# Kernel optimization log

Measured on AMD Instinct MI355X. Metric: run time of the kernel, lower is better.

## Reference

```python
import jax, jax.numpy as jnp
import numpy as np

N = 50000        # num_nodes
E = 200000       # num_edges
NODE_IN = 16
EDGE_IN = 8
H = 128          # hidden_dim (also per-head channels in GATConv)
HEADS = 4
L = 3            # num_layers
EPS = 1e-5
NEG_SLOPE = 0.2  # PyG GATConv default


def layer_norm(x, g, b):
    mu = jnp.mean(x, axis=-1, keepdims=True)
    v = jnp.var(x, axis=-1, keepdims=True)
    return (x - mu) * jax.lax.rsqrt(v + EPS) * g + b


def batch_norm_eval(x, g, b, rm, rv):
    return (x - rm) * jax.lax.rsqrt(rv + EPS) * g + b


def gat_layer(x, src, dst, W, a_src, a_dst, bias):
    # x: [N, H] -> per-head features [N, HEADS, H]
    xh = (x @ W).reshape(N, HEADS, H)
    al_src = jnp.sum(xh * a_src, axis=-1)  # [N, HEADS]
    al_dst = jnp.sum(xh * a_dst, axis=-1)  # [N, HEADS]
    alpha = jax.nn.leaky_relu(al_src[src] + al_dst[dst], NEG_SLOPE)  # [E', HEADS]
    # segment softmax over edges grouped by destination node
    m = jax.ops.segment_max(alpha, dst, num_segments=N)
    e = jnp.exp(alpha - m[dst])
    s = jax.ops.segment_sum(e, dst, num_segments=N)
    a = e / (s[dst] + 1e-16)
    msg = xh[src] * a[:, :, None]                 # [E', HEADS, H]
    out = jax.ops.segment_sum(msg, dst, num_segments=N)  # [N, HEADS, H]
    return jnp.mean(out, axis=1) + bias           # concat=False -> head mean


def setup_inputs() -> dict:
    key = jax.random.key(0)
    ks = jax.random.split(key, 24)
    s = 0.1
    inp = {
        "x": jax.random.normal(ks[0], (N, NODE_IN), jnp.float32),
        "edge_index": jax.random.randint(ks[1], (2, E), 0, N, jnp.int32),
        "edge_attr": jax.random.normal(ks[2], (E, EDGE_IN), jnp.float32),
        "shock_mask_nodes": jax.random.randint(ks[3], (N,), 0, 2, jnp.int32),
        # node encoder
        "enc_w": jax.random.normal(ks[4], (NODE_IN + 2, H), jnp.float32) * s,
        "enc_b": jnp.zeros((H,), jnp.float32),
        "enc_ln_g": jnp.ones((H,), jnp.float32),
        "enc_ln_b": jnp.zeros((H,), jnp.float32),
        # GAT layers (stacked over L)
        "gat_w": jax.random.normal(ks[5], (L, H, HEADS * H), jnp.float32) * s,
        "gat_att_src": jax.random.normal(ks[6], (L, HEADS, H), jnp.float32) * s,
        "gat_att_dst": jax.random.normal(ks[7], (L, HEADS, H), jnp.float32) * s,
        "gat_bias": jnp.zeros((L, H), jnp.float32),
        # BatchNorm (eval mode: running stats)
        "bn_g": jnp.ones((L, H), jnp.float32),
        "bn_b": jnp.zeros((L, H), jnp.float32),
        "bn_mean": jax.random.normal(ks[8], (L, H), jnp.float32) * 0.01,
        "bn_var": jnp.ones((L, H), jnp.float32),
        # edge MLP: (2H + EDGE_IN) -> H -> H//2 -> 1
        "em1_w": jax.random.normal(ks[9], (2 * H + EDGE_IN, H), jnp.float32) * s,
        "em1_b": jnp.zeros((H,), jnp.float32),
        "em_ln_g": jnp.ones((H,), jnp.float32),
        "em_ln_b": jnp.zeros((H,), jnp.float32),
        "em2_w": jax.random.normal(ks[10], (H, H // 2), jnp.float32) * s,
        "em2_b": jnp.zeros((H // 2,), jnp.float32),
        "em3_w": jax.random.normal(ks[11], (H // 2, 1), jnp.float32) * s,
        "em3_b": jnp.zeros((1,), jnp.float32),
    }
    return inp


def reference(x, edge_index, edge_attr, shock_mask_nodes,
              enc_w, enc_b, enc_ln_g, enc_ln_b,
              gat_w, gat_att_src, gat_att_dst, gat_bias,
              bn_g, bn_b, bn_mean, bn_var,
              em1_w, em1_b, em_ln_g, em_ln_b,
              em2_w, em2_b, em3_w, em3_b):
    src, dst = edge_index[0], edge_index[1]
    shock = shock_mask_nodes.astype(jnp.float32)[:, None]  # [N,1]
    # downstream indicator: scatter_add shock[src] into tgt, binarize
    down = jax.ops.segment_sum(shock[src, 0], dst, num_segments=N)
    down = (down > 0).astype(jnp.float32)[:, None]
    xa = jnp.concatenate([x, shock, down], axis=1)  # [N, NODE_IN+2]
    # node encoder (dropout off in eval)
    h = jax.nn.relu(layer_norm(xa @ enc_w + enc_b, enc_ln_g, enc_ln_b))
    # add self loops once (PyG GATConv default add_self_loops=True)
    loop = jnp.arange(N, dtype=src.dtype)
    src_sl = jnp.concatenate([src, loop])
    dst_sl = jnp.concatenate([dst, loop])
    for i in range(L):
        h = gat_layer(h, src_sl, dst_sl, gat_w[i], gat_att_src[i], gat_att_dst[i], gat_bias[i])
        h = batch_norm_eval(h, bn_g[i], bn_b[i], bn_mean[i], bn_var[i])
        if i < L - 1:
            h = jax.nn.relu(h)
    # edge predictor (note: source uses raw edge_attr, not augmented)
    edge_input = jnp.concatenate([h[src], h[dst], edge_attr], axis=1)  # [E, 2H+EDGE_IN]
    z = jax.nn.relu(layer_norm(edge_input @ em1_w + em1_b, em_ln_g, em_ln_b))
    z = jax.nn.relu(z @ em2_w + em2_b)
    delta = (z @ em3_w + em3_b)[:, 0]  # [E]
    return delta
```

## Files before the change

### kernel.cpp

```cpp
#include <hip/hip_runtime.h>
#include <hip/hip_bf16.h>


#define N_NODES 50000
#define N_EDGES 200000
#define ETOT    (N_EDGES + N_NODES)
#define HID     128
#define LN_EPS  1e-5f
#define NEG     0.2f
#define NSB     196

typedef __hip_bfloat16 bf16;
typedef __attribute__((ext_vector_type(8))) short v8s;
typedef __attribute__((ext_vector_type(4))) float v4f;
#define MFMA(a, b, c) __builtin_amdgcn_mfma_f32_16x16x32_bf16(a, b, c, 0, 0, 0)

__device__ __forceinline__ float b2f(unsigned short s) {
    return __uint_as_float(((unsigned int)s) << 16);
}
__device__ __forceinline__ unsigned short f2b(float f) {
    __hip_bfloat16 h = __float2bfloat16(f);
    return *reinterpret_cast<unsigned short*>(&h);
}
__device__ __forceinline__ unsigned int pack2(float a, float b) {
    return (unsigned int)f2b(a) | ((unsigned int)f2b(b) << 16);
}
__device__ __forceinline__ float pread(const void* p, size_t i, int isbf) {
    if (isbf) return b2f(((const unsigned short*)p)[i]);
    return ((const float*)p)[i];
}

__global__ void k_fill(float* out, int n, float v) {
    int i = blockIdx.x * blockDim.x + threadIdx.x;
    if (i < n) out[i] = v;
}

__global__ void k_detect(const unsigned short* __restrict__ xbuf,
                         int* __restrict__ flag) {
    int sane = 0;
    for (int j = threadIdx.x; j < 4096; j += 64) {
        unsigned short v = xbuf[2 * j];
        int e = (v >> 7) & 0xFF;
        if (v == 0 || (e > 96 && e < 160)) sane++;
    }
    for (int off = 32; off > 0; off >>= 1) sane += __shfl_down(sane, off);
    if (threadIdx.x == 0) flag[0] = (sane * 10 >= 4096 * 9) ? 1 : 0;
}

struct PrepArgs {
    const void *encw, *encb, *enlg, *enlb, *gatw, *asrc, *adst, *bias,
               *bng, *bnb, *bnm, *bnv, *em1w, *em1b, *emlg, *emlb,
               *em2w, *em2b, *em3w, *em3b;
};
#define PREP_ITEMS (150000 + 8193 + 1024 + 196608 + 32768 + 8192 + 3072 + 6144)
__global__ void k_prep(PrepArgs a, float* __restrict__ pool,
                       unsigned short* __restrict__ gwt,
                       unsigned short* __restrict__ uvt,
                       unsigned short* __restrict__ w2t,
                       float* __restrict__ wl,
                       unsigned short* __restrict__ wlhi,
                       unsigned short* __restrict__ wllo,
                       float* __restrict__ down, int* __restrict__ deg,
                       int* __restrict__ fill, const int* __restrict__ flag) {
    int i = blockIdx.x * 256 + threadIdx.x;
    int bf = flag[0];
    if (i < 150000) {
        int which = i / 50000, idx = i - which * 50000;
        if (which == 0) down[idx] = 0.f;
        else if (which == 1) deg[idx] = 0;
        else fill[idx] = 0;
        return;
    }
    i -= 150000;
    if (i < 8193) {
        const void* s; int off;
        if      (i < 2304) { s = a.encw; off = 0;    }
        else if (i < 2432) { s = a.encb; off = 2304; }
        else if (i < 2560) { s = a.enlg; off = 2432; }
        else if (i < 2688) { s = a.enlb; off = 2560; }
        else if (i < 4224) { s = a.asrc; off = 2688; }
        else if (i < 5760) { s = a.adst; off = 4224; }
        else if (i < 6144) { s = a.bias; off = 5760; }
        else if (i < 6528) { s = a.bng;  off = 6144; }
        else if (i < 6912) { s = a.bnb;  off = 6528; }
        else if (i < 7296) { s = a.bnm;  off = 6912; }
        else if (i < 7680) { s = a.bnv;  off = 7296; }
        else if (i < 7808) { s = a.em1b; off = 7680; }
        else if (i < 7936) { s = a.emlg; off = 7808; }
        else if (i < 8064) { s = a.emlb; off = 7936; }
        else if (i < 8128) { s = a.em2b; off = 8064; }
        else if (i < 8192) { s = a.em3w; off = 8128; }
        else               { s = a.em3b; off = 8192; }
        pool[i] = pread(s, i - off, bf);
        return;
    }
    i -= 8193;
    if (i < 1024) {
        int k = i >> 7, c = i & 127;
        pool[8200 + i] = pread(a.em1w, (size_t)(256 + k) * 128 + c, bf);
        return;
    }
    i -= 1024;
    if (i < 196608) {
        int L = i >> 16, rem = i & 65535, c = rem >> 9, k = rem & 511;
        gwt[i] = f2b(pread(a.gatw,
            (size_t)L * 65536 + (size_t)(k & 127) * 512 + (k >> 7) * 128 + c, bf));
        return;
    }
    i -= 196608;
    if (i < 32768) {
        int n = i >> 7, k = i & 127;
        float v = (n < 128) ? pread(a.em1w, (size_t)k * 128 + n, bf)
                            : pread(a.em1w, (size_t)(128 + k) * 128 + (n - 128), bf);
        uvt[i] = f2b(v);
        return;
    }
    i -= 32768;
    if (i < 8192) {
        int n = i >> 7, k = i & 127;
        w2t[i] = f2b(pread(a.em2w, (size_t)k * 64 + n, bf));
        return;
    }
    i -= 8192;
    if (i < 3072) {
        int L = i >> 10, rem = i & 1023, sd = rem >> 9, hh = (rem >> 7) & 3,
            kk = rem & 127;
        const void* av = sd ? a.adst : a.asrc;
        float acc = 0.f;
        for (int c = 0; c < 128; c++)
            acc += pread(a.gatw,
                       (size_t)L * 65536 + (size_t)kk * 512 + hh * 128 + c, bf)
                 * pread(av, (size_t)L * 512 + hh * 128 + c, bf);
        wl[i] = acc;
        return;
    }
    i -= 3072;
    if (i < 6144) {
        int L = i >> 11, rem = i & 2047, j = rem >> 7, kk = rem & 127;
        float d = 0.f;
        if (j < 8) {
            int sd = j >> 2, hh = j & 3;
            const void* av = sd ? a.adst : a.asrc;
            for (int c = 0; c < 128; c++)
                d += pread(a.gatw,
                         (size_t)L * 65536 + (size_t)kk * 512 + hh * 128 + c, bf)
                   * pread(av, (size_t)L * 512 + hh * 128 + c, bf);
        }
        unsigned short hi = f2b(d);
        wlhi[i] = hi;
        wllo[i] = f2b(d - b2f(hi));
    }
}

__global__ void k_graph(const int* __restrict__ ei, const int* __restrict__ shock,
                        float* __restrict__ down, int* __restrict__ deg) {
    int e = blockIdx.x * blockDim.x + threadIdx.x;
    if (e < ETOT) {
        int d = (e < N_EDGES) ? ei[N_EDGES + e] : (e - N_EDGES);
        atomicAdd(&deg[d], 1);
        if (e < N_EDGES && shock[ei[e]] != 0) down[d] = 1.f;
    }
}

__global__ __launch_bounds__(256) void k_scan1(
        const int* __restrict__ deg, int* __restrict__ bsum) {
    __shared__ int red[4];
    int b = blockIdx.x, t = threadIdx.x, lane = t & 63, w = t >> 6;
    int idx = b * 256 + t;
    int v = (idx < N_NODES) ? deg[idx] : 0;
#pragma unroll
    for (int off = 1; off < 64; off <<= 1) v += __shfl_xor(v, off);
    if (lane == 0) red[w] = v;
    __syncthreads();
    if (t == 0) bsum[b] = red[0] + red[1] + red[2] + red[3];
}

__global__ __launch_bounds__(256) void k_scan2(
        const int* __restrict__ deg, const int* __restrict__ bsum,
        int* __restrict__ row_start) {
    __shared__ int red[4];
    __shared__ int wsum[4];
    int b = blockIdx.x, t = threadIdx.x, lane = t & 63, w = t >> 6;
    int pv = (t < b) ? bsum[t] : 0;
    int sm = pv;
#pragma unroll
    for (int off = 1; off < 64; off <<= 1) sm += __shfl_xor(sm, off);
    if (lane == 0) red[w] = sm;
    int idx = b * 256 + t;
    int v = (idx < N_NODES) ? deg[idx] : 0;
    int inc = v;
#pragma unroll
    for (int off = 1; off < 64; off <<= 1) {
        int u = __shfl_up(inc, off);
        if (lane >= off) inc += u;
    }
    if (lane == 63) wsum[w] = inc;
    __syncthreads();
    int boff = red[0] + red[1] + red[2] + red[3];
    int wo = 0;
#pragma unroll
    for (int i = 0; i < 4; i++) if (i < w) wo += wsum[i];
    if (idx < N_NODES) row_start[idx] = boff + wo + (inc - v);
    if (b == 0 && t == 0) row_start[N_NODES] = ETOT;
}

__global__ void k_csr(const int* __restrict__ ei, const int* __restrict__ row_start,
                      int* __restrict__ fill, int* __restrict__ csr_src) {
    int e = blockIdx.x * blockDim.x + threadIdx.x;
    if (e < ETOT) {
        int s, d;
        if (e < N_EDGES) { s = ei[e]; d = ei[N_EDGES + e]; }
        else             { s = e - N_EDGES; d = s; }
        int pos = row_start[d] + atomicAdd(&fill[d], 1);
        csr_src[pos] = s;
    }
}

__global__ __launch_bounds__(256) void k_encoder(
        const void* __restrict__ xraw, const int* __restrict__ flag,
        const int* __restrict__ shock, const float* __restrict__ down,
        const float* __restrict__ enc_w, const float* __restrict__ enc_b,
        const float* __restrict__ ln_g, const float* __restrict__ ln_b,
        unsigned short* __restrict__ h) {
    __shared__ float sw[2304];
    __shared__ float sp[384];
    int t = threadIdx.x;
    for (int i = t; i < 2304; i += 256) sw[i] = enc_w[i];
    if (t < 128)      sp[t] = enc_b[t];
    else if (t < 256) sp[t] = ln_g[t - 128];
    if (t < 128)      sp[256 + t] = ln_b[t];
    __syncthreads();

    int w = t >> 6, l = t & 63;
    int n = blockIdx.x * 4 + w;
    int bf = flag[0];
    int c0 = 2 * l, c1 = c0 + 1;

    float xv = (l < 16) ? pread(xraw, (size_t)n * 16 + l, bf) : 0.f;
    float xs = (float)shock[n];
    float xd = down[n];

    float a0 = sp[c0], a1 = sp[c1];
#pragma unroll
    for (int k = 0; k < 16; k++) {
        float xk = __shfl(xv, k);
        a0 = fmaf(xk, sw[k * HID + c0], a0);
        a1 = fmaf(xk, sw[k * HID + c1], a1);
    }
    a0 = fmaf(xs, sw[16 * HID + c0], a0); a1 = fmaf(xs, sw[16 * HID + c1], a1);
    a0 = fmaf(xd, sw[17 * HID + c0], a0); a1 = fmaf(xd, sw[17 * HID + c1], a1);

    float s = a0 + a1, q = a0 * a0 + a1 * a1;
#pragma unroll
    for (int off = 1; off < 64; off <<= 1) {
        s += __shfl_xor(s, off);
        q += __shfl_xor(q, off);
    }
    float mu = s * (1.f / 128.f);
    float var = q * (1.f / 128.f) - mu * mu;
    float rstd = rsqrtf(var + LN_EPS);
    float v0 = fmaxf((a0 - mu) * rstd * sp[128 + c0] + sp[256 + c0], 0.f);
    float v1 = fmaxf((a1 - mu) * rstd * sp[128 + c1] + sp[256 + c1], 0.f);
    *(unsigned int*)&h[(size_t)n * HID + c0] = pack2(v0, v1);
}

__global__ __launch_bounds__(256) void k_logits(
        const unsigned short* __restrict__ h, const float* __restrict__ wl,
        float* __restrict__ al_s, float* __restrict__ al_d) {
    __shared__ float wls[1024];
    int t = threadIdx.x;
    for (int i = t; i < 1024; i += 256) wls[i] = wl[i];
    __syncthreads();
    int lane = t & 63, w = t >> 6, l15 = lane & 15, q = lane >> 4;
    int n = blockIdx.x * 16 + w * 4 + q;
    v8s hv = *(const v8s*)&h[(size_t)n * 128 + l15 * 8];
    float hf[8];
#pragma unroll
    for (int m = 0; m < 8; m++) hf[m] = b2f((unsigned short)hv[m]);
    float p[8] = {};
#pragma unroll
    for (int j = 0; j < 8; j++) {
        float4 wa = *(const float4*)&wls[j * 128 + l15 * 8];
        float4 wb = *(const float4*)&wls[j * 128 + l15 * 8 + 4];
        p[j] = fmaf(hf[0], wa.x, p[j]); p[j] = fmaf(hf[1], wa.y, p[j]);
        p[j] = fmaf(hf[2], wa.z, p[j]); p[j] = fmaf(hf[3], wa.w, p[j]);
        p[j] = fmaf(hf[4], wb.x, p[j]); p[j] = fmaf(hf[5], wb.y, p[j]);
        p[j] = fmaf(hf[6], wb.z, p[j]); p[j] = fmaf(hf[7], wb.w, p[j]);
    }
#pragma unroll
    for (int off = 1; off < 16; off <<= 1)
#pragma unroll
        for (int j = 0; j < 8; j++) p[j] += __shfl_xor(p[j], off);
    if (l15 == 0) {
        float4 vs = {p[0], p[1], p[2], p[3]};
        float4 vd = {p[4], p[5], p[6], p[7]};
        *(float4*)&al_s[n * 4] = vs;
        *(float4*)&al_d[n * 4] = vd;
    }
}

__global__ __launch_bounds__(256) void k_agg4(
        const unsigned short* __restrict__ h, const float* __restrict__ al_src,
        const float* __restrict__ al_dst,
        const int* __restrict__ row_start, const int* __restrict__ csr_src,
        unsigned short* __restrict__ agg) {
    int w = threadIdx.x >> 6, l = threadIdx.x & 63;
    int n = blockIdx.x * 4 + w;
    int g = l >> 4, c = l & 15;
    int r0 = row_start[n], r1 = row_start[n + 1];
    int last = r1 - 1;
    int iters = (r1 - r0 + 3) >> 2;
    float4 ad4 = *(const float4*)&al_dst[n * 4];
    float s0 = 0.f, s1 = 0.f, s2 = 0.f, s3 = 0.f;
    float acc[4][8] = {};

    int j0 = r0 + g;
    int vC = (j0 <= last) ? 1 : 0;
    int jc = vC ? j0 : last;
    int iC = csr_src[jc];
    float4 aC = *(const float4*)&al_src[iC * 4];
    v8s hC = *(const v8s*)&h[(size_t)iC * 128 + c * 8];

#pragma unroll 1
    for (int it = 0; it < iters; it++) {
        float4 aN = aC; v8s hN = hC; int vN = 0;
        if (it + 1 < iters) {
            int jn = r0 + (it + 1) * 4 + g;
            vN = (jn <= last) ? 1 : 0;
            jn = vN ? jn : last;
            int iN = csr_src[jn];
            aN = *(const float4*)&al_src[iN * 4];
            hN = *(const v8s*)&h[(size_t)iN * 128 + c * 8];
        }
        float t0 = aC.x + ad4.x; t0 = (t0 >= 0.f) ? t0 : NEG * t0;
        float t1 = aC.y + ad4.y; t1 = (t1 >= 0.f) ? t1 : NEG * t1;
        float t2 = aC.z + ad4.z; t2 = (t2 >= 0.f) ? t2 : NEG * t2;
        float t3 = aC.w + ad4.w; t3 = (t3 >= 0.f) ? t3 : NEG * t3;
        float m = (float)vC;
        float e0 = __expf(t0) * m, e1 = __expf(t1) * m,
              e2 = __expf(t2) * m, e3 = __expf(t3) * m;
        s0 += e0; s1 += e1; s2 += e2; s3 += e3;
#pragma unroll
        for (int i = 0; i < 8; i++) {
            float hv = b2f((unsigned short)hC[i]);
            acc[0][i] = fmaf(e0, hv, acc[0][i]);
            acc[1][i] = fmaf(e1, hv, acc[1][i]);
            acc[2][i] = fmaf(e2, hv, acc[2][i]);
            acc[3][i] = fmaf(e3, hv, acc[3][i]);
        }
        aC = aN; hC = hN; vC = vN;
    }
    s0 += __shfl_xor(s0, 16); s0 += __shfl_xor(s0, 32);
    s1 += __shfl_xor(s1, 16); s1 += __shfl_xor(s1, 32);
    s2 += __shfl_xor(s2, 16); s2 += __shfl_xor(s2, 32);
    s3 += __shfl_xor(s3, 16); s3 += __shfl_xor(s3, 32);
#pragma unroll
    for (int hh = 0; hh < 4; hh++)
#pragma unroll
        for (int i = 0; i < 8; i++) {
            acc[hh][i] += __shfl_xor(acc[hh][i], 16);
            acc[hh][i] += __shfl_xor(acc[hh][i], 32);
        }
    float sg = (g == 0) ? s0 : (g == 1) ? s1 : (g == 2) ? s2 : s3;
    float inv = 1.f / (sg + 1e-16f);
    short o[8];
#pragma unroll
    for (int i = 0; i < 8; i++) {
        float av = (g == 0) ? acc[0][i] : (g == 1) ? acc[1][i]
                 : (g == 2) ? acc[2][i] : acc[3][i];
        o[i] = (short)f2b(av * inv);
    }
    *(v8s*)&agg[(size_t)n * 512 + g * 128 + c * 8] = *(const v8s*)o;
}

__global__ __launch_bounds__(256, 4) void k_gemm2(
        const unsigned short* __restrict__ A,
        const unsigned short* __restrict__ Wt,
        const float* __restrict__ bias,
        const float* __restrict__ bn_g, const float* __restrict__ bn_b,
        const float* __restrict__ bn_m, const float* __restrict__ bn_v,
        unsigned short* __restrict__ hout, int relu_flag,
        const unsigned short* __restrict__ wlhi,
        const unsigned short* __restrict__ wllo,
        float* __restrict__ al_s, float* __restrict__ al_d, int logit_flag) {
    __shared__ __align__(16) unsigned short As[2][64 * 136];
    int t = threadIdx.x;
    int lane = t & 63, w = t >> 6, l15 = lane & 15, q = lane >> 4;
    int m0 = blockIdx.x * 64;
    int c0 = w * 32 + 2 * l15, c1 = c0 + 1;

    v8s st[4];
#pragma unroll
    for (int it = 0; it < 4; it++) {
        int cc = t + it * 256, row = cc >> 4, ch = cc & 15;
        v8s val = {0, 0, 0, 0, 0, 0, 0, 0};
        if (m0 + row < N_NODES)
            val = *(const v8s*)&A[(size_t)(m0 + row) * 512 + ch * 8];
        st[it] = val;
    }
#pragma unroll
    for (int it = 0; it < 4; it++) {
        int cc = t + it * 256, row = cc >> 4, ch = cc & 15;
        *(v8s*)&As[0][row * 136 + ch * 8] = st[it];
    }
    __syncthreads();

    v4f acc[4][2] = {};
#pragma unroll
    for (int kc = 0; kc < 4; kc++) {
        if (kc < 3) {
#pragma unroll
            for (int it = 0; it < 4; it++) {
                int cc = t + it * 256, row = cc >> 4, ch = cc & 15;
                v8s val = {0, 0, 0, 0, 0, 0, 0, 0};
                if (m0 + row < N_NODES)
                    val = *(const v8s*)&A[(size_t)(m0 + row) * 512
                                          + (kc + 1) * 128 + ch * 8];
                st[it] = val;
            }
        }
#pragma unroll
        for (int kt = 0; kt < 4; kt++) {
            v8s b0 = *(const v8s*)&Wt[(size_t)c0 * 512 + kc * 128 + kt * 32 + q * 8];
            v8s b1 = *(const v8s*)&Wt[(size_t)c1 * 512 + kc * 128 + kt * 32 + q * 8];
#pragma unroll
            for (int mt = 0; mt < 4; mt++) {
                v8s a = *(const v8s*)&As[kc & 1][(mt * 16 + l15) * 136
                                                 + kt * 32 + q * 8];
                acc[mt][0] = MFMA(a, b0, acc[mt][0]);
                acc[mt][1] = MFMA(a, b1, acc[mt][1]);
            }
        }
        if (kc < 3) {
#pragma unroll
            for (int it = 0; it < 4; it++) {
                int cc = t + it * 256, row = cc >> 4, ch = cc & 15;
                *(v8s*)&As[(kc + 1) & 1][row * 136 + ch * 8] = st[it];
            }
        }
        __syncthreads();
    }

    float bi0 = bias[c0], bi1 = bias[c1];
    float sc0 = rsqrtf(bn_v[c0] + LN_EPS) * bn_g[c0];
    float sc1 = rsqrtf(bn_v[c1] + LN_EPS) * bn_g[c1];
    float sh0 = bn_b[c0] - bn_m[c0] * sc0;
    float sh1 = bn_b[c1] - bn_m[c1] * sc1;
#pragma unroll
    for (int mt = 0; mt < 4; mt++)
#pragma unroll
        for (int r = 0; r < 4; r++) {
            int row = mt * 16 + q * 4 + r;
            int node = m0 + row;
            float v0 = (0.25f * acc[mt][0][r] + bi0) * sc0 + sh0;
            float v1 = (0.25f * acc[mt][1][r] + bi1) * sc1 + sh1;
            if (relu_flag) { v0 = fmaxf(v0, 0.f); v1 = fmaxf(v1, 0.f); }
            unsigned int pv = pack2(v0, v1);
            if (node < N_NODES)
                *(unsigned int*)&hout[(size_t)node * 128 + c0] = pv;
            if (logit_flag)
                *(unsigned int*)&As[0][row * 136 + c0] = pv;
        }

    if (logit_flag) {
        __syncthreads();
        v4f accL = {0.f, 0.f, 0.f, 0.f};
#pragma unroll
        for (int kt = 0; kt < 4; kt++) {
            v8s a  = *(const v8s*)&As[0][(w * 16 + l15) * 136 + kt * 32 + q * 8];
            v8s bh = *(const v8s*)&wlhi[(size_t)l15 * 128 + kt * 32 + q * 8];
            v8s bl = *(const v8s*)&wllo[(size_t)l15 * 128 + kt * 32 + q * 8];
            accL = MFMA(a, bh, accL);
            accL = MFMA(a, bl, accL);
        }
        if (l15 < 8) {
#pragma unroll
            for (int r = 0; r < 4; r++) {
                int node = m0 + w * 16 + q * 4 + r;
                if (node < N_NODES) {
                    if (l15 < 4) al_s[node * 4 + l15] = accL[r];
                    else         al_d[node * 4 + (l15 - 4)] = accL[r];
                }
            }
        }
    }
}

__global__ __launch_bounds__(256, 4) void k_uvgemm(
        const unsigned short* __restrict__ A, const unsigned short* __restrict__ Wt,
        unsigned short* __restrict__ UV) {
    __shared__ __align__(16) unsigned short As[64 * 136];
    int t = threadIdx.x;
    int lane = t & 63, w = t >> 6, l15 = lane & 15, q = lane >> 4;
    int m0 = blockIdx.x * 64, n0 = blockIdx.y * 128;
    int c0 = n0 + w * 32 + 2 * l15;

    v8s b[2][4];
#pragma unroll
    for (int nt = 0; nt < 2; nt++)
#pragma unroll
        for (int kt = 0; kt < 4; kt++)
            b[nt][kt] = *(const v8s*)&Wt[(size_t)(c0 + nt) * 128 + kt * 32 + q * 8];
#pragma unroll
    for (int it = 0; it < 4; it++) {
        int c = t + it * 256;
        int row = c >> 4, ch = c & 15;
        v8s val = {0, 0, 0, 0, 0, 0, 0, 0};
        if (m0 + row < N_NODES)
            val = *(const v8s*)&A[(size_t)(m0 + row) * 128 + ch * 8];
        *(v8s*)&As[row * 136 + ch * 8] = val;
    }
    __syncthreads();

    v4f acc[4][2] = {};
#pragma unroll
    for (int kt = 0; kt < 4; kt++)
#pragma unroll
        for (int mt = 0; mt < 4; mt++) {
            v8s a = *(const v8s*)&As[(mt * 16 + l15) * 136 + kt * 32 + q * 8];
            acc[mt][0] = MFMA(a, b[0][kt], acc[mt][0]);
            acc[mt][1] = MFMA(a, b[1][kt], acc[mt][1]);
        }
#pragma unroll
    for (int mt = 0; mt < 4; mt++)
#pragma unroll
        for (int r = 0; r < 4; r++) {
            int node = m0 + mt * 16 + q * 4 + r;
            if (node < N_NODES)
                *(unsigned int*)&UV[(size_t)node * 256 + c0] =
                    pack2(acc[mt][0][r], acc[mt][1][r]);
        }
}

__global__ __launch_bounds__(256) void k_edgemlp3(
        const unsigned short* __restrict__ UV, const int* __restrict__ ei,
        const void* __restrict__ eraw, const int* __restrict__ flag,
        const float* __restrict__ w1e, const float* __restrict__ em1b,
        const float* __restrict__ lng, const float* __restrict__ lnb,
        const unsigned short* __restrict__ w2t, const float* __restrict__ em2b,
        const float* __restrict__ em3w, const float* __restrict__ em3b,
        float* __restrict__ out) {
    __shared__ __align__(16) unsigned short za[64 * 136];
    __shared__ __align__(16) float w1e_s[1024];
    __shared__ __align__(16) unsigned short ea_s[64 * 8];
    __shared__ int idx_s[128];
    __shared__ float part[4][64];

    int t = threadIdx.x;
    int lane = t & 63, w = t >> 6, l15 = lane & 15, q = lane >> 4;
    int e0 = blockIdx.x * 64;
    int bf = flag[0];
    int cb = l15 * 8;

    float bc[8], lg[8], lb[8];
#pragma unroll
    for (int j = 0; j < 8; j++) {
        bc[j] = em1b[cb + j];
        lg[j] = lng[cb + j];
        lb[j] = lnb[cb + j];
    }

    for (int i = t; i < 1024; i += 256) w1e_s[i] = w1e[i];
    if (t < 64) {
        idx_s[t * 2]     = ei[e0 + t];
        idx_s[t * 2 + 1] = ei[N_EDGES + e0 + t];
        if (bf) {
            *(v8s*)&ea_s[t * 8] =
                *(const v8s*)((const unsigned short*)eraw + (size_t)(e0 + t) * 8);
        } else {
            short tmp[8];
#pragma unroll
            for (int j = 0; j < 8; j++)
                tmp[j] = (short)f2b(((const float*)eraw)[(size_t)(e0 + t) * 8 + j]);
            *(v8s*)&ea_s[t * 8] = *(const v8s*)tmp;
        }
    }
    __syncthreads();

#pragma unroll 1
    for (int i = 0; i < 4; i++) {
        int el = w * 16 + i * 4 + q;
        int src = idx_s[el * 2], dst = idx_s[el * 2 + 1];
        v8s uu = *(const v8s*)&UV[(size_t)src * 256 + cb];
        v8s vv = *(const v8s*)&UV[(size_t)dst * 256 + 128 + cb];
        v8s ea8 = *(const v8s*)&ea_s[el * 8];
        float eaf[8];
#pragma unroll
        for (int k = 0; k < 8; k++) eaf[k] = b2f((unsigned short)ea8[k]);
        float e[8] = {};
#pragma unroll
        for (int k = 0; k < 8; k++) {
            float4 wa = *(const float4*)&w1e_s[k * 128 + cb];
            float4 wb = *(const float4*)&w1e_s[k * 128 + cb + 4];
            e[0] = fmaf(eaf[k], wa.x, e[0]);
            e[1] = fmaf(eaf[k], wa.y, e[1]);
            e[2] = fmaf(eaf[k], wa.z, e[2]);
            e[3] = fmaf(eaf[k], wa.w, e[3]);
            e[4] = fmaf(eaf[k], wb.x, e[4]);
            e[5] = fmaf(eaf[k], wb.y, e[5]);
            e[6] = fmaf(eaf[k], wb.z, e[6]);
            e[7] = fmaf(eaf[k], wb.w, e[7]);
        }
        float z[8];
        float s = 0.f, qq = 0.f;
#pragma unroll
        for (int j = 0; j < 8; j++) {
            float zz = b2f((unsigned short)uu[j]) + b2f((unsigned short)vv[j])
                     + e[j] + bc[j];
            z[j] = zz;
            s += zz;
            qq = fmaf(zz, zz, qq);
        }
#pragma unroll
        for (int off = 1; off < 16; off <<= 1) {
            s  += __shfl_xor(s, off);
            qq += __shfl_xor(qq, off);
        }
        float mu = s * (1.f / 128.f);
        float var = qq * (1.f / 128.f) - mu * mu;
        float rstd = rsqrtf(var + LN_EPS);
        short o[8];
#pragma unroll
        for (int j = 0; j < 8; j++)
            o[j] = (short)f2b(fmaxf((z[j] - mu) * rstd * lg[j] + lb[j], 0.f));
        *(v8s*)&za[el * 136 + cb] = *(const v8s*)o;
    }
    __syncthreads();

    v8s b2[4];
#pragma unroll
    for (int kt = 0; kt < 4; kt++)
        b2[kt] = *(const v8s*)&w2t[(size_t)(w * 16 + l15) * 128 + kt * 32 + q * 8];
    v4f acc2[4] = {};
#pragma unroll
    for (int kt = 0; kt < 4; kt++)
#pragma unroll
        for (int mt = 0; mt < 4; mt++) {
            v8s a = *(const v8s*)&za[(mt * 16 + l15) * 136 + kt * 32 + q * 8];
            acc2[mt] = MFMA(a, b2[kt], acc2[mt]);
        }

    {
        int col = w * 16 + l15;
        float b2c = em2b[col], w3c = em3w[col];
#pragma unroll
        for (int mt = 0; mt < 4; mt++)
#pragma unroll
            for (int r = 0; r < 4; r++) {
                float vv = fmaxf(acc2[mt][r] + b2c, 0.f) * w3c;
#pragma unroll
                for (int off = 1; off < 16; off <<= 1) vv += __shfl_xor(vv, off);
                if (l15 == 0) part[w][mt * 16 + q * 4 + r] = vv;
            }
    }
    __syncthreads();
    if (t < 64)
        out[e0 + t] = part[0][t] + part[1][t] + part[2][t] + part[3][t]
                    + em3b[0];
}

extern "C" __attribute__((visibility("default")))
void kernel_launch(void* const* d_in, const int* in_sizes, int n_in,
                   void* d_out, int out_size, void* d_ws, size_t ws_size,
                   hipStream_t stream) {
    float* out = (float*)d_out;

    static const int EXP_SIZES[24] = {
        800000, 400000, 1600000, 50000, 2304, 128, 128, 128,
        196608, 1536, 1536, 384, 384, 384, 384, 384,
        33792, 128, 128, 128, 8192, 64, 64, 1};
    bool ok = (n_in == 24) && (out_size == N_EDGES);
    if (ok) for (int i = 0; i < 24; i++) ok = ok && (in_sizes[i] == EXP_SIZES[i]);
    if (!ok) {
        k_fill<<<(out_size + 255) / 256, 256, 0, stream>>>(out, out_size, 4.0f);
        return;
    }
    if (ws_size < (size_t)68000000) {
        k_fill<<<(out_size + 255) / 256, 256, 0, stream>>>(out, out_size, 8.0f);
        return;
    }

    const int* ei    = (const int*)d_in[1];
    const int* shock = (const int*)d_in[3];

    char* ws = (char*)d_ws;
    unsigned short* h_bf  = (unsigned short*)(ws + 0);
    unsigned short* agg   = (unsigned short*)(ws + 12800000);
    unsigned short* UV    = agg;
    float* al_s    = (float*)(ws + 64000000);
    float* al_d    = (float*)(ws + 64800000);
    float* down    = (float*)(ws + 65600000);
    int*   deg     = (int*)  (ws + 65800000);
    int*   row_st  = (int*)  (ws + 66000000);
    int*   fill    = (int*)  (ws + 66200064);
    int*   csr_src = (int*)  (ws + 66400064);
    int*   flag    = (int*)  (ws + 67400064);
    unsigned short* gwt = (unsigned short*)(ws + 67400128);
    unsigned short* uvt = (unsigned short*)(ws + 67793344);
    unsigned short* w2t = (unsigned short*)(ws + 67858880);
    float* pool    = (float*)(ws + 67875264);
    int*   bsum    = (int*)  (ws + 67912160);
    float* wl      = (float*)(ws + 67912960);
    unsigned short* wlhi = (unsigned short*)(ws + 67925248);
    unsigned short* wllo = (unsigned short*)(ws + 67937536);

    float* cencw = pool + 0;    float* cencb = pool + 2304;
    float* cenlg = pool + 2432; float* cenlb = pool + 2560;
    float* cbias = pool + 5760; float* cbng  = pool + 6144;
    float* cbnb  = pool + 6528; float* cbnm  = pool + 6912;
    float* cbnv  = pool + 7296; float* cem1b = pool + 7680;
    float* cemlg = pool + 7808; float* cemlb = pool + 7936;
    float* cem2b = pool + 8064; float* cem3w = pool + 8128;
    float* cem3b = pool + 8192;
    float* w1e   = pool + 8200;

    k_detect<<<1, 64, 0, stream>>>((const unsigned short*)d_in[0], flag);

    PrepArgs pa;
    pa.encw = d_in[4];  pa.encb = d_in[5];  pa.enlg = d_in[6];  pa.enlb = d_in[7];
    pa.gatw = d_in[8];  pa.asrc = d_in[9];  pa.adst = d_in[10]; pa.bias = d_in[11];
    pa.bng  = d_in[12]; pa.bnb  = d_in[13]; pa.bnm  = d_in[14]; pa.bnv  = d_in[15];
    pa.em1w = d_in[16]; pa.em1b = d_in[17]; pa.emlg = d_in[18]; pa.emlb = d_in[19];
    pa.em2w = d_in[20]; pa.em2b = d_in[21]; pa.em3w = d_in[22]; pa.em3b = d_in[23];
    k_prep<<<(PREP_ITEMS + 255) / 256, 256, 0, stream>>>(
        pa, pool, gwt, uvt, w2t, wl, wlhi, wllo, down, deg, fill, flag);

    k_graph<<<(ETOT + 255) / 256, 256, 0, stream>>>(ei, shock, down, deg);
    k_scan1<<<NSB, 256, 0, stream>>>(deg, bsum);
    k_scan2<<<NSB, 256, 0, stream>>>(deg, bsum, row_st);
    k_csr<<<(ETOT + 255) / 256, 256, 0, stream>>>(ei, row_st, fill, csr_src);
    k_encoder<<<N_NODES / 4, 256, 0, stream>>>(
        d_in[0], flag, shock, down, cencw, cencb, cenlg, cenlb, h_bf);
    k_logits<<<N_NODES / 16, 256, 0, stream>>>(h_bf, wl, al_s, al_d);
    for (int i = 0; i < 3; i++) {
        k_agg4<<<N_NODES / 4, 256, 0, stream>>>(
            h_bf, al_s, al_d, row_st, csr_src, agg);
        k_gemm2<<<782, 256, 0, stream>>>(
            agg, gwt + (size_t)i * 65536,
            cbias + i * 128, cbng + i * 128, cbnb + i * 128,
            cbnm + i * 128, cbnv + i * 128, h_bf, (i < 2) ? 1 : 0,
            wlhi + (size_t)(i + 1) * 2048, wllo + (size_t)(i + 1) * 2048,
            al_s, al_d, (i < 2) ? 1 : 0);
    }
    k_uvgemm<<<dim3(782, 2), 256, 0, stream>>>(h_bf, uvt, UV);
    k_edgemlp3<<<N_EDGES / 64, 256, 0, stream>>>(
        UV, ei, d_in[2], flag, w1e, cem1b, cemlg, cemlb,
        w2t, cem2b, cem3w, cem3b, out);
}
```

Before: 477.9 us.

## Shrink edge-MLP block to 16 edges and trim prep attention-weight work

The edge MLP kernel now handles 16 edges per 256-thread block instead of 64, so each 16-lane group processes one edge in a single pass rather than looping four times. The second-layer MFMA runs one M tile instead of four. This gives four times as many blocks to expose more parallelism and shorten the per-block serial gather loop. The cost is reloading the 4KB w1e table and the w2t fragments per block, which is four times the redundant weight traffic. The prep kernel also stops computing unused layer-1/2 logit weights and the zero padding rows via dot products; those rows are now written directly.

```diff
diff --git a/kernel.cpp b/kernel.cpp
--- a/kernel.cpp
+++ b/kernel.cpp
@@ -52,7 +52,7 @@
                *bng, *bnb, *bnm, *bnv, *em1w, *em1b, *emlg, *emlb,
                *em2w, *em2b, *em3w, *em3b;
 };
-#define PREP_ITEMS (150000 + 8193 + 1024 + 196608 + 32768 + 8192 + 3072 + 6144)
+#define PREP_ITEMS (150000 + 8193 + 1024 + 196608 + 32768 + 8192 + 1024 + 2048 + 2048)
 __global__ void k_prep(PrepArgs a, float* __restrict__ pool,
                        unsigned short* __restrict__ gwt,
                        unsigned short* __restrict__ uvt,
@@ -122,33 +122,36 @@
         return;
     }
     i -= 8192;
-    if (i < 3072) {
-        int L = i >> 10, rem = i & 1023, sd = rem >> 9, hh = (rem >> 7) & 3,
-            kk = rem & 127;
+    if (i < 1024) {
+        int sd = i >> 9, hh = (i >> 7) & 3, kk = i & 127;
         const void* av = sd ? a.adst : a.asrc;
         float acc = 0.f;
         for (int c = 0; c < 128; c++)
-            acc += pread(a.gatw,
-                       (size_t)L * 65536 + (size_t)kk * 512 + hh * 128 + c, bf)
-                 * pread(av, (size_t)L * 512 + hh * 128 + c, bf);
+            acc += pread(a.gatw, (size_t)kk * 512 + hh * 128 + c, bf)
+                 * pread(av, hh * 128 + c, bf);
         wl[i] = acc;
         return;
     }
-    i -= 3072;
-    if (i < 6144) {
-        int L = i >> 11, rem = i & 2047, j = rem >> 7, kk = rem & 127;
+    i -= 1024;
+    if (i < 2048) {
+        int L = 1 + (i >> 10), rem = i & 1023, j = rem >> 7, kk = rem & 127;
+        int sd = j >> 2, hh = j & 3;
+        const void* av = sd ? a.adst : a.asrc;
         float d = 0.f;
-        if (j < 8) {
-            int sd = j >> 2, hh = j & 3;
-            const void* av = sd ? a.adst : a.asrc;
-            for (int c = 0; c < 128; c++)
-                d += pread(a.gatw,
-                         (size_t)L * 65536 + (size_t)kk * 512 + hh * 128 + c, bf)
-                   * pread(av, (size_t)L * 512 + hh * 128 + c, bf);
-        }
+        for (int c = 0; c < 128; c++)
+            d += pread(a.gatw,
+                     (size_t)L * 65536 + (size_t)kk * 512 + hh * 128 + c, bf)
+               * pread(av, (size_t)L * 512 + hh * 128 + c, bf);
         unsigned short hi = f2b(d);
-        wlhi[i] = hi;
-        wllo[i] = f2b(d - b2f(hi));
+        wlhi[L * 2048 + j * 128 + kk] = hi;
+        wllo[L * 2048 + j * 128 + kk] = f2b(d - b2f(hi));
+        return;
+    }
+    i -= 2048;
+    if (i < 2048) {
+        int L = 1 + (i >> 10), rem = i & 1023, j = 8 + (rem >> 7), kk = rem & 127;
+        wlhi[L * 2048 + j * 128 + kk] = 0;
+        wllo[L * 2048 + j * 128 + kk] = 0;
     }
 }
 
@@ -532,7 +535,7 @@
         }
 }
 
-__global__ __launch_bounds__(256) void k_edgemlp3(
+__global__ __launch_bounds__(256) void k_edgemlp4(
         const unsigned short* __restrict__ UV, const int* __restrict__ ei,
         const void* __restrict__ eraw, const int* __restrict__ flag,
         const float* __restrict__ w1e, const float* __restrict__ em1b,
@@ -540,28 +543,21 @@
         const unsigned short* __restrict__ w2t, const float* __restrict__ em2b,
         const float* __restrict__ em3w, const float* __restrict__ em3b,
         float* __restrict__ out) {
-    __shared__ __align__(16) unsigned short za[64 * 136];
+    __shared__ __align__(16) unsigned short za[16 * 136];
     __shared__ __align__(16) float w1e_s[1024];
-    __shared__ __align__(16) unsigned short ea_s[64 * 8];
-    __shared__ int idx_s[128];
-    __shared__ float part[4][64];
+    __shared__ __align__(16) unsigned short ea_s[16 * 8];
+    __shared__ int idx_s[32];
+    __shared__ float part[4][16];
 
     int t = threadIdx.x;
     int lane = t & 63, w = t >> 6, l15 = lane & 15, q = lane >> 4;
-    int e0 = blockIdx.x * 64;
+    int g = t >> 4;
+    int e0 = blockIdx.x * 16;
     int bf = flag[0];
     int cb = l15 * 8;
 
-    float bc[8], lg[8], lb[8];
-#pragma unroll
-    for (int j = 0; j < 8; j++) {
-        bc[j] = em1b[cb + j];
-        lg[j] = lng[cb + j];
-        lb[j] = lnb[cb + j];
-    }
-
     for (int i = t; i < 1024; i += 256) w1e_s[i] = w1e[i];
-    if (t < 64) {
+    if (t < 16) {
         idx_s[t * 2]     = ei[e0 + t];
         idx_s[t * 2 + 1] = ei[N_EDGES + e0 + t];
         if (bf) {
@@ -577,13 +573,19 @@
     }
     __syncthreads();
 
-#pragma unroll 1
-    for (int i = 0; i < 4; i++) {
-        int el = w * 16 + i * 4 + q;
-        int src = idx_s[el * 2], dst = idx_s[el * 2 + 1];
+    {
+        int src = idx_s[g * 2], dst = idx_s[g * 2 + 1];
         v8s uu = *(const v8s*)&UV[(size_t)src * 256 + cb];
         v8s vv = *(const v8s*)&UV[(size_t)dst * 256 + 128 + cb];
-        v8s ea8 = *(const v8s*)&ea_s[el * 8];
+        v8s ea8 = *(const v8s*)&ea_s[g * 8];
+
+        float bc[8], lg[8], lb[8];
+#pragma unroll
+        for (int j = 0; j < 8; j++) {
+            bc[j] = em1b[cb + j];
+            lg[j] = lng[cb + j];
+            lb[j] = lnb[cb + j];
+        }
         float eaf[8];
 #pragma unroll
         for (int k = 0; k < 8; k++) eaf[k] = b2f((unsigned short)ea8[k]);
@@ -623,38 +625,34 @@
 #pragma unroll
         for (int j = 0; j < 8; j++)
             o[j] = (short)f2b(fmaxf((z[j] - mu) * rstd * lg[j] + lb[j], 0.f));
-        *(v8s*)&za[el * 136 + cb] = *(const v8s*)o;
-    }
-    __syncthreads();
-
-    v8s b2[4];
+        *(v8s*)&za[g * 136 + cb] = *(const v8s*)o;
+    }
+    __syncthreads();
+
+    v8s b2v[4];
 #pragma unroll
     for (int kt = 0; kt < 4; kt++)
-        b2[kt] = *(const v8s*)&w2t[(size_t)(w * 16 + l15) * 128 + kt * 32 + q * 8];
-    v4f acc2[4] = {};
-#pragma unroll
-    for (int kt = 0; kt < 4; kt++)
-#pragma unroll
-        for (int mt = 0; mt < 4; mt++) {
-            v8s a = *(const v8s*)&za[(mt * 16 + l15) * 136 + kt * 32 + q * 8];
-            acc2[mt] = MFMA(a, b2[kt], acc2[mt]);
-        }
+        b2v[kt] = *(const v8s*)&w2t[(size_t)(w * 16 + l15) * 128 + kt * 32 + q * 8];
+    v4f acc2 = {0.f, 0.f, 0.f, 0.f};
+#pragma unroll
+    for (int kt = 0; kt < 4; kt++) {
+        v8s a = *(const v8s*)&za[l15 * 136 + kt * 32 + q * 8];
+        acc2 = MFMA(a, b2v[kt], acc2);
+    }
 
     {
         int col = w * 16 + l15;
         float b2c = em2b[col], w3c = em3w[col];
 #pragma unroll
-        for (int mt = 0; mt < 4; mt++)
-#pragma unroll
-            for (int r = 0; r < 4; r++) {
-                float vv = fmaxf(acc2[mt][r] + b2c, 0.f) * w3c;
-#pragma unroll
-                for (int off = 1; off < 16; off <<= 1) vv += __shfl_xor(vv, off);
-                if (l15 == 0) part[w][mt * 16 + q * 4 + r] = vv;
-            }
-    }
-    __syncthreads();
-    if (t < 64)
+        for (int r = 0; r < 4; r++) {
+            float vv2 = fmaxf(acc2[r] + b2c, 0.f) * w3c;
+#pragma unroll
+            for (int off = 1; off < 16; off <<= 1) vv2 += __shfl_xor(vv2, off);
+            if (l15 == 0) part[w][q * 4 + r] = vv2;
+        }
+    }
+    __syncthreads();
+    if (t < 16)
         out[e0 + t] = part[0][t] + part[1][t] + part[2][t] + part[3][t]
                     + em3b[0];
 }
@@ -743,7 +741,7 @@
             al_s, al_d, (i < 2) ? 1 : 0);
     }
     k_uvgemm<<<dim3(782, 2), 256, 0, stream>>>(h_bf, uvt, UV);
-    k_edgemlp3<<<N_EDGES / 64, 256, 0, stream>>>(
+    k_edgemlp4<<<N_EDGES / 16, 256, 0, stream>>>(
         UV, ei, d_in[2], flag, w1e, cem1b, cemlg, cemlb,
         w2t, cem2b, cem3w, cem3b, out);
 }
```

Result: no change. 480.5 us (+0.5%).
